# Optimization experiments

Hardware: AMD Instinct MI355X
Metric: run time of the kernel (lower is better)

The kernel has to match this reference:

```python
import jax, jax.numpy as jnp
import numpy as np

EPS = 1e-10
B, S, D, K = 8, 2048, 512, 1024
TEMP = 1.0  # quantizer temperature set to 1.0 in SQVAE.__init__


def _ln(x, g, b):
    m = x.mean(-1, keepdims=True)
    v = x.var(-1, keepdims=True)
    return (x - m) / jnp.sqrt(v + 1e-5) * g + b


def _mlp(x, w1, b1, g1, be1, w2, b2, g2, be2):
    # feed_forward: Linear -> ReLU -> LayerNorm, twice (MLPLayers=2)
    h = _ln(jax.nn.relu(x @ w1 + b1), g1, be1)
    return _ln(jax.nn.relu(h @ w2 + b2), g2, be2)


def setup_inputs() -> dict:
    key = jax.random.key(0)
    ks = jax.random.split(key, 20)
    W = 0.04  # small init scale to keep distances / softmax well-conditioned
    p = lambda k, sh, s=1.0: jax.random.normal(k, sh, dtype=jnp.float32) * s
    return {
        'x': p(ks[0], (B, S, D)),
        'gumbel_u': jax.random.uniform(ks[1], (B * S, K), dtype=jnp.float32),
        'enc_w1': p(ks[2], (D, D), W), 'enc_b1': jnp.zeros(D, jnp.float32),
        'enc_g1': jnp.ones(D, jnp.float32), 'enc_be1': jnp.zeros(D, jnp.float32),
        'enc_w2': p(ks[3], (D, D), W), 'enc_b2': jnp.zeros(D, jnp.float32),
        'enc_g2': jnp.ones(D, jnp.float32), 'enc_be2': jnp.zeros(D, jnp.float32),
        'dec_w1': p(ks[4], (D, D), W), 'dec_b1': jnp.zeros(D, jnp.float32),
        'dec_g1': jnp.ones(D, jnp.float32), 'dec_be1': jnp.zeros(D, jnp.float32),
        'dec_w2': p(ks[5], (D, D), W), 'dec_b2': jnp.zeros(D, jnp.float32),
        'dec_g2': jnp.ones(D, jnp.float32), 'dec_be2': jnp.zeros(D, jnp.float32),
        'codebook': p(ks[6], (K, D)),
        'log_param_q': jnp.zeros((), jnp.float32),
    }


def reference(x, gumbel_u, enc_w1, enc_b1, enc_g1, enc_be1, enc_w2, enc_b2, enc_g2, enc_be2,
              dec_w1, dec_b1, dec_g1, dec_be1, dec_w2, dec_b2, dec_g2, dec_be2,
              codebook, log_param_q):
    bs, seq, d = x.shape
    z = _mlp(x, enc_w1, enc_b1, enc_g1, enc_be1, enc_w2, enc_b2, enc_g2, enc_be2)
    # gaussian_1: log_var_q = 0 -> var_q = exp(log_param_q_scalar)
    var_q = jnp.exp(log_param_q)
    w = 0.5 / jnp.clip(var_q, 1e-10)  # 0.5 * precision_q (scalar)
    zf = z.reshape(-1, d)  # [N, D]
    # cdist^2 style distance, scaled by weight -> logits [N, K]
    dist = w * (jnp.sum(zf * zf, axis=1, keepdims=True)
                + jnp.sum(codebook * codebook, axis=1)
                - 2.0 * zf @ codebook.T)
    logit = -dist
    logp = jax.nn.log_softmax(logit, axis=-1)
    probs = jnp.exp(logp)
    # gumbel-softmax sample (train path), noise provided as uniform input
    g = -jnp.log(-jnp.log(gumbel_u + EPS) + EPS)
    encodings = jax.nn.softmax((logit + g) / TEMP, axis=-1)
    z_q = (encodings @ codebook).reshape(bs, seq, d)
    kld_discrete = jnp.sum(probs * logp) / bs
    kld_continuous = jnp.mean(jnp.sum((z - z_q) ** 2 * w, axis=(1, 2)))
    loss = kld_discrete + kld_continuous
    avg_probs = jnp.mean(jax.lax.stop_gradient(probs), axis=0)
    perplexity = jnp.exp(-jnp.sum(avg_probs * jnp.log(avg_probs + 1e-7)))
    x_rec = _mlp(z_q, dec_w1, dec_b1, dec_g1, dec_be1, dec_w2, dec_b2, dec_g2, dec_be2)
    return x_rec, loss, perplexity
```

## Files before the change

### kernel.cpp

```cpp
#include <hip/hip_runtime.h>
#include <math.h>

#define NROWS 16384
#define DIM   512
#define KCODE 1024

typedef __attribute__((ext_vector_type(8))) __bf16 bf16x8;
typedef __attribute__((ext_vector_type(4))) float f32x4;

__device__ __forceinline__ float wave_reduce_sum(float v) {
  #pragma unroll
  for (int m = 1; m < 64; m <<= 1) v += __shfl_xor(v, m, 64);
  return v;
}
__device__ __forceinline__ float wave_reduce_max(float v) {
  #pragma unroll
  for (int m = 1; m < 64; m <<= 1) v = fmaxf(v, __shfl_xor(v, m, 64));
  return v;
}
__device__ __forceinline__ unsigned short f2bf(float f) {
  union { float f; unsigned u; } v; v.f = f;
  unsigned r = v.u + 0x7FFFu + ((v.u >> 16) & 1u);
  return (unsigned short)(r >> 16);
}
__device__ __forceinline__ float bf2f(unsigned short h) {
  union { unsigned u; float f; } v; v.u = ((unsigned)h) << 16;
  return v.f;
}
__device__ __forceinline__ uint4 pack8(const float* x) {
  uint4 r;
  r.x = (unsigned)f2bf(x[0]) | ((unsigned)f2bf(x[1]) << 16);
  r.y = (unsigned)f2bf(x[2]) | ((unsigned)f2bf(x[3]) << 16);
  r.z = (unsigned)f2bf(x[4]) | ((unsigned)f2bf(x[5]) << 16);
  r.w = (unsigned)f2bf(x[6]) | ((unsigned)f2bf(x[7]) << 16);
  return r;
}

__device__ __forceinline__ void glds16(const void* g, void* lds) {
  __builtin_amdgcn_global_load_lds(
      (const __attribute__((address_space(1))) unsigned int*)g,
      (__attribute__((address_space(3))) unsigned int*)lds, 16, 0, 0);
}

template <int NPASS, int EPI, int K, int N, int LDA, int MROWS>
__global__ __launch_bounds__(512, 2) void gemm256(
    const unsigned short* A0, const unsigned short* A1, const unsigned short* A2,
    const unsigned short* B0, const unsigned short* B1, const unsigned short* B2,
    const float* __restrict__ znorm, const float* __restrict__ cnorm,
    const float* __restrict__ lpq,
    const unsigned short* __restrict__ zh, const unsigned short* __restrict__ zl,
    float* __restrict__ kldc,
    unsigned short* __restrict__ outb, float* __restrict__ outf) {
  __shared__ char smem[65536];
  const int t = threadIdx.x;
  const int l = t & 63, w = t >> 6;
  const int wm = w >> 2, wn = w & 3;
  const int NTN = N / 256;
  const int b = blockIdx.x;
  const int xcd = b & 7, j = b >> 3;
  const int MT_PER_XCD = (MROWS / 256) / 8;
  const int m0 = (xcd * MT_PER_XCD + j / NTN) * 256;
  const int n0 = (j % NTN) * 256;

  f32x4 acc[8][4];
  #pragma unroll
  for (int i = 0; i < 8; ++i)
    #pragma unroll
    for (int jj = 0; jj < 4; ++jj) acc[i][jj] = (f32x4){0.f, 0.f, 0.f, 0.f};

  const int row_lo = w * 16 + (l & 15);
  const int row_hi = (w + 8) * 16 + (l & 15);
  const int kcol = (l >> 4) * 8;
  const int dA0 = w * 1024;
  const int dA1 = (w + 8) * 1024;
  const int dB0 = 16384 + w * 1024;
  const int dB1 = 16384 + (w + 8) * 1024;

  const size_t oA0 = (size_t)(m0 + row_lo) * LDA + kcol;
  const size_t oA1 = (size_t)(m0 + row_hi) * LDA + kcol;
  const size_t oB0 = (size_t)(n0 + row_lo) * K + kcol;
  const size_t oB1 = (size_t)(n0 + row_hi) * K + kcol;

  constexpr int SPP = K / 32;
  constexpr int NSTEP = NPASS * SPP;

  auto issue = [&](int ss) {
    const int p = (NPASS == 1) ? 0 : (ss / SPP);
    const int kt = (ss % SPP) * 32;
    const unsigned short* A = (p == 0) ? A0 : (p == 1) ? A1 : A2;
    const unsigned short* B = (p == 0) ? B0 : (p == 1) ? B1 : B2;
    char* hb = smem + (ss & 1) * 32768;
    glds16(A + oA0 + kt, hb + dA0);
    glds16(A + oA1 + kt, hb + dA1);
    glds16(B + oB0 + kt, hb + dB0);
    glds16(B + oB1 + kt, hb + dB1);
  };

  issue(0);
  #pragma unroll 1
  for (int s = 0; s < NSTEP; ++s) {
    if (s + 1 < NSTEP) {
      issue(s + 1);
      asm volatile("s_waitcnt vmcnt(4)" ::: "memory");
    } else {
      asm volatile("s_waitcnt vmcnt(0)" ::: "memory");
    }
    __builtin_amdgcn_s_barrier();
    const char* hb = smem + (s & 1) * 32768;
    bf16x8 af[8], bfr[4];
    #pragma unroll
    for (int i = 0; i < 4; ++i)
      bfr[i] = *(const bf16x8*)(hb + 16384 + (wn * 4 + i) * 1024 + l * 16);
    #pragma unroll
    for (int i = 0; i < 8; ++i)
      af[i] = *(const bf16x8*)(hb + (wm * 8 + i) * 1024 + l * 16);
    #pragma unroll
    for (int mi = 0; mi < 8; ++mi)
      #pragma unroll
      for (int ni = 0; ni < 4; ++ni)
        acc[mi][ni] = __builtin_amdgcn_mfma_f32_16x16x32_bf16(af[mi], bfr[ni], acc[mi][ni], 0, 0, 0);
    __builtin_amdgcn_s_barrier();
  }

  float* slab = (float*)(smem + w * 4352);
  const int q = l >> 4, c16 = l & 15;
  const int c4 = (l & 15) * 4;
  const float wq = 0.5f / fmaxf(expf(lpq[0]), 1e-10f);
  float local = 0.f;

  #pragma unroll
  for (int mi = 0; mi < 8; ++mi) {
    __syncthreads();
    #pragma unroll
    for (int ni = 0; ni < 4; ++ni)
      #pragma unroll
      for (int r = 0; r < 4; ++r)
        slab[(q * 4 + r) * 68 + ni * 16 + c16] = acc[mi][ni][r];
    __syncthreads();
    #pragma unroll
    for (int pp = 0; pp < 4; ++pp) {
      const int row = pp * 4 + q;
      const float4 v4 = *(const float4*)&slab[row * 68 + c4];
      float v[4] = {v4.x, v4.y, v4.z, v4.w};
      const int m = m0 + wm * 128 + mi * 16 + row;
      const int nc = n0 + wn * 64 + c4;
      if (EPI == 1) {
        const float zn = znorm[m];
        const float4 cn = *(const float4*)&cnorm[nc];
        float4 o;
        o.x = -wq * (zn + cn.x - 2.f * v[0]);
        o.y = -wq * (zn + cn.y - 2.f * v[1]);
        o.z = -wq * (zn + cn.z - 2.f * v[2]);
        o.w = -wq * (zn + cn.w - 2.f * v[3]);
        *(float4*)&outf[(size_t)m * N + nc] = o;
      } else {
        const uint2 h2 = *(const uint2*)&zh[(size_t)m * N + nc];
        const uint2 l2 = *(const uint2*)&zl[(size_t)m * N + nc];
        const float z0 = bf2f((unsigned short)(h2.x & 0xFFFF)) + bf2f((unsigned short)(l2.x & 0xFFFF));
        const float z1 = bf2f((unsigned short)(h2.x >> 16))    + bf2f((unsigned short)(l2.x >> 16));
        const float z2 = bf2f((unsigned short)(h2.y & 0xFFFF)) + bf2f((unsigned short)(l2.y & 0xFFFF));
        const float z3 = bf2f((unsigned short)(h2.y >> 16))    + bf2f((unsigned short)(l2.y >> 16));
        const float d0 = z0 - v[0], d1 = z1 - v[1], d2 = z2 - v[2], d3 = z3 - v[3];
        local += d0 * d0 + d1 * d1 + d2 * d2 + d3 * d3;
        uint2 st;
        st.x = (unsigned)f2bf(v[0]) | ((unsigned)f2bf(v[1]) << 16);
        st.y = (unsigned)f2bf(v[2]) | ((unsigned)f2bf(v[3]) << 16);
        *(uint2*)&outb[(size_t)m * N + nc] = st;
      }
    }
  }
  if (EPI == 2) {
    local = wave_reduce_sum(local) * wq;
    if (l == 0) atomicAdd(kldc, local);
  }
}

template <int NPASS, int EPI, int K, int N, int LDA>
__global__ __launch_bounds__(256) void gemm_bt(
    const unsigned short* A0, const unsigned short* A1, const unsigned short* A2,
    const unsigned short* B0, const unsigned short* B1, const unsigned short* B2,
    const float* __restrict__ bias,
    const float* __restrict__ znorm, const float* __restrict__ cnorm,
    const float* __restrict__ lpq,
    const unsigned short* __restrict__ zh, const unsigned short* __restrict__ zl,
    float* __restrict__ kldc,
    unsigned short* __restrict__ outb, float* __restrict__ outf) {
  __shared__ char smem[32768];
  const int t = threadIdx.x;
  const int l = t & 63, w = t >> 6;
  const int wm = w >> 1, wn = w & 1;
  const int NTN = N / 128;
  const int b = blockIdx.x;
  const int xcd = b & 7;
  const int j = b >> 3;
  const int m0 = (xcd * 16 + j / NTN) * 128;
  const int n0 = (j % NTN) * 128;

  f32x4 acc[4][4];
  #pragma unroll
  for (int i = 0; i < 4; ++i)
    #pragma unroll
    for (int jj = 0; jj < 4; ++jj) acc[i][jj] = (f32x4){0.f, 0.f, 0.f, 0.f};

  const int row_lo = w * 16 + (l & 15);
  const int row_hi = (w + 4) * 16 + (l & 15);
  const int kcol = (l >> 4) * 8;
  const int dA0 = w * 1024;
  const int dA1 = (w + 4) * 1024;
  const int dB0 = 8192 + w * 1024;
  const int dB1 = 8192 + (w + 4) * 1024;

  const size_t oA0 = (size_t)(m0 + row_lo) * LDA + kcol;
  const size_t oA1 = (size_t)(m0 + row_hi) * LDA + kcol;
  const size_t oB0 = (size_t)(n0 + row_lo) * K + kcol;
  const size_t oB1 = (size_t)(n0 + row_hi) * K + kcol;

  constexpr int SPP = K / 32;
  constexpr int NSTEP = NPASS * SPP;

  auto issue = [&](int ss) {
    const int p = (NPASS == 1) ? 0 : (ss / SPP);
    const int kt = (ss % SPP) * 32;
    const unsigned short* A = (p == 0) ? A0 : (p == 1) ? A1 : A2;
    const unsigned short* B = (p == 0) ? B0 : (p == 1) ? B1 : B2;
    char* hb = smem + (ss & 1) * 16384;
    glds16(A + oA0 + kt, hb + dA0);
    glds16(A + oA1 + kt, hb + dA1);
    glds16(B + oB0 + kt, hb + dB0);
    glds16(B + oB1 + kt, hb + dB1);
  };

  issue(0);
  #pragma unroll 1
  for (int s = 0; s < NSTEP; ++s) {
    if (s + 1 < NSTEP) {
      issue(s + 1);
      asm volatile("s_waitcnt vmcnt(4)" ::: "memory");
    } else {
      asm volatile("s_waitcnt vmcnt(0)" ::: "memory");
    }
    __builtin_amdgcn_s_barrier();
    const char* hb = smem + (s & 1) * 16384;
    bf16x8 af[4], bfr[4];
    #pragma unroll
    for (int i = 0; i < 4; ++i) {
      af[i]  = *(const bf16x8*)(hb + (wm * 4 + i) * 1024 + l * 16);
      bfr[i] = *(const bf16x8*)(hb + 8192 + (wn * 4 + i) * 1024 + l * 16);
    }
    #pragma unroll
    for (int mi = 0; mi < 4; ++mi)
      #pragma unroll
      for (int ni = 0; ni < 4; ++ni)
        acc[mi][ni] = __builtin_amdgcn_mfma_f32_16x16x32_bf16(af[mi], bfr[ni], acc[mi][ni], 0, 0, 0);
    __builtin_amdgcn_s_barrier();
  }

  float* slab = (float*)(smem + w * 4352);
  const int q = l >> 4, c16 = l & 15;
  const int c4 = (l & 15) * 4;
  const float wq = (EPI >= 1) ? 0.5f / fmaxf(expf(lpq[0]), 1e-10f) : 0.f;
  float local = 0.f;

  #pragma unroll
  for (int mi = 0; mi < 4; ++mi) {
    __syncthreads();
    #pragma unroll
    for (int ni = 0; ni < 4; ++ni)
      #pragma unroll
      for (int r = 0; r < 4; ++r)
        slab[(q * 4 + r) * 68 + ni * 16 + c16] = acc[mi][ni][r];
    __syncthreads();
    #pragma unroll
    for (int pp = 0; pp < 4; ++pp) {
      const int row = pp * 4 + q;
      const float4 v4 = *(const float4*)&slab[row * 68 + c4];
      float v[4] = {v4.x, v4.y, v4.z, v4.w};
      const int m = m0 + wm * 64 + mi * 16 + row;
      const int nc = n0 + wn * 64 + c4;
      if (EPI == 0) {
        const float4 b4 = *(const float4*)&bias[nc];
        v[0] = fmaxf(v[0] + b4.x, 0.f);
        v[1] = fmaxf(v[1] + b4.y, 0.f);
        v[2] = fmaxf(v[2] + b4.z, 0.f);
        v[3] = fmaxf(v[3] + b4.w, 0.f);
        uint2 st;
        st.x = (unsigned)f2bf(v[0]) | ((unsigned)f2bf(v[1]) << 16);
        st.y = (unsigned)f2bf(v[2]) | ((unsigned)f2bf(v[3]) << 16);
        *(uint2*)&outb[(size_t)m * N + nc] = st;
      } else if (EPI == 1) {
        const float zn = znorm[m];
        const float4 cn = *(const float4*)&cnorm[nc];
        float4 o;
        o.x = -wq * (zn + cn.x - 2.f * v[0]);
        o.y = -wq * (zn + cn.y - 2.f * v[1]);
        o.z = -wq * (zn + cn.z - 2.f * v[2]);
        o.w = -wq * (zn + cn.w - 2.f * v[3]);
        *(float4*)&outf[(size_t)m * N + nc] = o;
      } else {
        const uint2 h2 = *(const uint2*)&zh[(size_t)m * N + nc];
        const uint2 l2 = *(const uint2*)&zl[(size_t)m * N + nc];
        const float z0 = bf2f((unsigned short)(h2.x & 0xFFFF)) + bf2f((unsigned short)(l2.x & 0xFFFF));
        const float z1 = bf2f((unsigned short)(h2.x >> 16))    + bf2f((unsigned short)(l2.x >> 16));
        const float z2 = bf2f((unsigned short)(h2.y & 0xFFFF)) + bf2f((unsigned short)(l2.y & 0xFFFF));
        const float z3 = bf2f((unsigned short)(h2.y >> 16))    + bf2f((unsigned short)(l2.y >> 16));
        const float d0 = z0 - v[0], d1 = z1 - v[1], d2 = z2 - v[2], d3 = z3 - v[3];
        local += d0 * d0 + d1 * d1 + d2 * d2 + d3 * d3;
        uint2 st;
        st.x = (unsigned)f2bf(v[0]) | ((unsigned)f2bf(v[1]) << 16);
        st.y = (unsigned)f2bf(v[2]) | ((unsigned)f2bf(v[3]) << 16);
        *(uint2*)&outb[(size_t)m * N + nc] = st;
      }
    }
  }
  if (EPI == 2) {
    local = wave_reduce_sum(local) * wq;
    if (l == 0) atomicAdd(kldc, local);
  }
}

template <int MODE>
__global__ __launch_bounds__(256) void ln_rows(
    const unsigned short* __restrict__ X, const float* __restrict__ g,
    const float* __restrict__ be, unsigned short* __restrict__ Y,
    unsigned short* __restrict__ Yl, float* __restrict__ znorm,
    float* __restrict__ Yf) {
  const int l = threadIdx.x & 63, wv = threadIdx.x >> 6;
  float gv[8], bv[8];
  {
    const float4 a = *(const float4*)&g[l * 8];
    const float4 b = *(const float4*)&g[l * 8 + 4];
    gv[0] = a.x; gv[1] = a.y; gv[2] = a.z; gv[3] = a.w;
    gv[4] = b.x; gv[5] = b.y; gv[6] = b.z; gv[7] = b.w;
    const float4 c = *(const float4*)&be[l * 8];
    const float4 d = *(const float4*)&be[l * 8 + 4];
    bv[0] = c.x; bv[1] = c.y; bv[2] = c.z; bv[3] = c.w;
    bv[4] = d.x; bv[5] = d.y; bv[6] = d.z; bv[7] = d.w;
  }
  const int row0 = blockIdx.x * 32 + wv * 8;
  for (int rr = 0; rr < 8; ++rr) {
    const int row = row0 + rr;
    const uint4 raw = *(const uint4*)&X[(size_t)row * 512 + l * 8];
    float v[8];
    const unsigned rw[4] = {raw.x, raw.y, raw.z, raw.w};
    #pragma unroll
    for (int i = 0; i < 4; ++i) {
      v[2 * i]     = bf2f((unsigned short)(rw[i] & 0xFFFF));
      v[2 * i + 1] = bf2f((unsigned short)(rw[i] >> 16));
    }
    float s = 0.f, ss = 0.f;
    #pragma unroll
    for (int i = 0; i < 8; ++i) { s += v[i]; ss += v[i] * v[i]; }
    #pragma unroll
    for (int m = 1; m < 64; m <<= 1) {
      s += __shfl_xor(s, m, 64);
      ss += __shfl_xor(ss, m, 64);
    }
    const float mean = s * (1.f / 512.f);
    const float var = ss * (1.f / 512.f) - mean * mean;
    const float rstd = rsqrtf(var + 1e-5f);
    float y[8];
    #pragma unroll
    for (int i = 0; i < 8; ++i) y[i] = (v[i] - mean) * rstd * gv[i] + bv[i];
    if (MODE == 0) {
      *(uint4*)&Y[(size_t)row * 512 + l * 8] = pack8(y);
    } else if (MODE == 1) {
      float lo[8], ns = 0.f;
      unsigned short hx[8];
      #pragma unroll
      for (int i = 0; i < 8; ++i) {
        hx[i] = f2bf(y[i]);
        lo[i] = y[i] - bf2f(hx[i]);
        ns += y[i] * y[i];
      }
      uint4 hv;
      hv.x = (unsigned)hx[0] | ((unsigned)hx[1] << 16);
      hv.y = (unsigned)hx[2] | ((unsigned)hx[3] << 16);
      hv.z = (unsigned)hx[4] | ((unsigned)hx[5] << 16);
      hv.w = (unsigned)hx[6] | ((unsigned)hx[7] << 16);
      *(uint4*)&Y[(size_t)row * 512 + l * 8] = hv;
      *(uint4*)&Yl[(size_t)row * 512 + l * 8] = pack8(lo);
      ns = wave_reduce_sum(ns);
      if (l == 0) znorm[row] = ns;
    } else {
      float4 o0, o1;
      o0.x = y[0]; o0.y = y[1]; o0.z = y[2]; o0.w = y[3];
      o1.x = y[4]; o1.y = y[5]; o1.z = y[6]; o1.w = y[7];
      *(float4*)&Yf[(size_t)row * 512 + l * 8] = o0;
      *(float4*)&Yf[(size_t)row * 512 + l * 8 + 4] = o1;
    }
  }
}

__global__ __launch_bounds__(256) void convert_f32_bf16(
    const float* __restrict__ X, unsigned short* __restrict__ Y) {
  const size_t i = ((size_t)blockIdx.x * 256 + threadIdx.x) * 8;
  const float4 a = *(const float4*)&X[i];
  const float4 b = *(const float4*)&X[i + 4];
  float v[8] = {a.x, a.y, a.z, a.w, b.x, b.y, b.z, b.w};
  *(uint4*)&Y[i] = pack8(v);
}

__global__ __launch_bounds__(256) void prep_cb(
    const float* __restrict__ CB, unsigned short* __restrict__ H,
    unsigned short* __restrict__ L, float* __restrict__ cnorm) {
  const int wv = threadIdx.x >> 6, l = threadIdx.x & 63;
  const int r = blockIdx.x * 4 + wv;
  const float* row = &CB[(size_t)r * 512 + l * 8];
  const float4 a = *(const float4*)row;
  const float4 b = *(const float4*)(row + 4);
  float x[8] = {a.x, a.y, a.z, a.w, b.x, b.y, b.z, b.w};
  float s = 0.f, lo[8];
  unsigned short hi[8];
  #pragma unroll
  for (int i = 0; i < 8; ++i) {
    s += x[i] * x[i];
    hi[i] = f2bf(x[i]);
    lo[i] = x[i] - bf2f(hi[i]);
  }
  uint4 hv;
  hv.x = (unsigned)hi[0] | ((unsigned)hi[1] << 16);
  hv.y = (unsigned)hi[2] | ((unsigned)hi[3] << 16);
  hv.z = (unsigned)hi[4] | ((unsigned)hi[5] << 16);
  hv.w = (unsigned)hi[6] | ((unsigned)hi[7] << 16);
  *(uint4*)&H[(size_t)r * 512 + l * 8] = hv;
  *(uint4*)&L[(size_t)r * 512 + l * 8] = pack8(lo);
  s = wave_reduce_sum(s);
  if (l == 0) cnorm[r] = s;
}

__global__ __launch_bounds__(256) void transpose_f32_bf16(
    const float* __restrict__ in, unsigned short* __restrict__ out, int R, int C) {
  __shared__ float tile[32][33];
  const int ntc = C >> 5;
  const int c0 = (blockIdx.x % ntc) * 32, r0 = (blockIdx.x / ntc) * 32;
  const int tx = threadIdx.x & 31, ty = threadIdx.x >> 5;
  #pragma unroll
  for (int i = 0; i < 4; ++i)
    tile[ty + 8 * i][tx] = in[(size_t)(r0 + ty + 8 * i) * C + c0 + tx];
  __syncthreads();
  #pragma unroll
  for (int i = 0; i < 4; ++i)
    out[(size_t)(c0 + ty + 8 * i) * R + r0 + tx] = f2bf(tile[tx][ty + 8 * i]);
}

__global__ __launch_bounds__(256) void softmax_gumbel(
    const float* logits, const float* __restrict__ U, unsigned short* E,
    float* __restrict__ colsum, float* __restrict__ kldd_acc) {
  __shared__ float cs[1024];
  __shared__ float kd[4];
  const int t = threadIdx.x;
  const int wv = t >> 6, l = t & 63;
  #pragma unroll
  for (int i = 0; i < 4; ++i) cs[t + 256 * i] = 0.f;
  __syncthreads();
  float psum[16];
  #pragma unroll
  for (int i = 0; i < 16; ++i) psum[i] = 0.f;
  float kldd = 0.f;
  const int nbase = blockIdx.x * 16 + wv * 4;

  for (int it = 0; it < 4; ++it) {
    const int row = nbase + it;
    const size_t off = (size_t)row * KCODE + 4 * l;
    float v[16];
    #pragma unroll
    for (int jj = 0; jj < 4; ++jj) {
      const float4 t4 = *(const float4*)&logits[off + 256 * jj];
      v[4 * jj + 0] = t4.x; v[4 * jj + 1] = t4.y; v[4 * jj + 2] = t4.z; v[4 * jj + 3] = t4.w;
    }
    float m = v[0];
    #pragma unroll
    for (int i = 1; i < 16; ++i) m = fmaxf(m, v[i]);
    m = wave_reduce_max(m);
    float se = 0.f;
    #pragma unroll
    for (int i = 0; i < 16; ++i) se += expf(v[i] - m);
    se = wave_reduce_sum(se);
    const float lz = logf(se);
    float pl = 0.f;
    #pragma unroll
    for (int i = 0; i < 16; ++i) {
      const float lp = v[i] - m - lz;
      const float p = expf(lp);
      psum[i] += p;
      pl += p * lp;
    }
    kldd += pl;
    float y[16];
    #pragma unroll
    for (int jj = 0; jj < 4; ++jj) {
      const float4 t4 = *(const float4*)&U[off + 256 * jj];
      y[4 * jj + 0] = v[4 * jj + 0] - logf(-logf(t4.x + 1e-10f) + 1e-10f);
      y[4 * jj + 1] = v[4 * jj + 1] - logf(-logf(t4.y + 1e-10f) + 1e-10f);
      y[4 * jj + 2] = v[4 * jj + 2] - logf(-logf(t4.z + 1e-10f) + 1e-10f);
      y[4 * jj + 3] = v[4 * jj + 3] - logf(-logf(t4.w + 1e-10f) + 1e-10f);
    }
    float m2 = y[0];
    #pragma unroll
    for (int i = 1; i < 16; ++i) m2 = fmaxf(m2, y[i]);
    m2 = wave_reduce_max(m2);
    float s2 = 0.f;
    #pragma unroll
    for (int i = 0; i < 16; ++i) s2 += expf(y[i] - m2);
    s2 = wave_reduce_sum(s2);
    const float inv = 1.f / s2;
    #pragma unroll
    for (int jj = 0; jj < 4; ++jj) {
      ushort4 e;
      e.x = f2bf(expf(y[4 * jj + 0] - m2) * inv);
      e.y = f2bf(expf(y[4 * jj + 1] - m2) * inv);
      e.z = f2bf(expf(y[4 * jj + 2] - m2) * inv);
      e.w = f2bf(expf(y[4 * jj + 3] - m2) * inv);
      *(ushort4*)&E[(size_t)row * 2048 + 4 * l + 256 * jj] = e;
    }
  }
  #pragma unroll
  for (int jj = 0; jj < 4; ++jj)
    #pragma unroll
    for (int c = 0; c < 4; ++c)
      atomicAdd(&cs[256 * jj + 4 * l + c], psum[4 * jj + c]);
  kldd = wave_reduce_sum(kldd);
  if (l == 0) kd[wv] = kldd;
  __syncthreads();
  #pragma unroll
  for (int i = 0; i < 4; ++i) {
    const float vv = cs[t + 256 * i];
    if (vv != 0.f) atomicAdd(&colsum[t + 256 * i], vv);
  }
  if (t == 0) atomicAdd(kldd_acc, kd[0] + kd[1] + kd[2] + kd[3]);
}

__global__ __launch_bounds__(256) void finalize(
    const float* __restrict__ colsum, const float* __restrict__ scal,
    float* __restrict__ out) {
  const int t = threadIdx.x;
  float ent = 0.f;
  #pragma unroll
  for (int jj = 0; jj < 4; ++jj) {
    const float a = colsum[t + 256 * jj] * (1.f / 16384.f);
    ent += a * logf(a + 1e-7f);
  }
  ent = wave_reduce_sum(ent);
  __shared__ float red[4];
  if ((t & 63) == 0) red[t >> 6] = ent;
  __syncthreads();
  if (t == 0) {
    const float tot = red[0] + red[1] + red[2] + red[3];
    out[0] = (scal[0] + scal[1]) * (1.f / 8.f);
    out[1] = expf(-tot);
  }
}

extern "C" void kernel_launch(void* const* d_in, const int* in_sizes, int n_in,
                              void* d_out, int out_size, void* d_ws, size_t ws_size,
                              hipStream_t stream) {
  const float* x      = (const float*)d_in[0];
  const float* gu     = (const float*)d_in[1];
  const float* enc_w1 = (const float*)d_in[2];
  const float* enc_b1 = (const float*)d_in[3];
  const float* enc_g1 = (const float*)d_in[4];
  const float* enc_e1 = (const float*)d_in[5];
  const float* enc_w2 = (const float*)d_in[6];
  const float* enc_b2 = (const float*)d_in[7];
  const float* enc_g2 = (const float*)d_in[8];
  const float* enc_e2 = (const float*)d_in[9];
  const float* dec_w1 = (const float*)d_in[10];
  const float* dec_b1 = (const float*)d_in[11];
  const float* dec_g1 = (const float*)d_in[12];
  const float* dec_e1 = (const float*)d_in[13];
  const float* dec_w2 = (const float*)d_in[14];
  const float* dec_b2 = (const float*)d_in[15];
  const float* dec_g2 = (const float*)d_in[16];
  const float* dec_e2 = (const float*)d_in[17];
  const float* cb     = (const float*)d_in[18];
  const float* lpq    = (const float*)d_in[19];
  float* out = (float*)d_out;
  char* wsb = (char*)d_ws;

  float*          logits = (float*)(wsb + 0);
  unsigned short* Eb     = (unsigned short*)(wsb + 0);
  unsigned short* t1     = (unsigned short*)(wsb + 67108864);
  unsigned short* xb     = (unsigned short*)(wsb + 83886080);
  unsigned short* zh     = xb;
  unsigned short* hq     = (unsigned short*)(wsb + 100663296);
  unsigned short* zl     = (unsigned short*)(wsb + 117440512);
  unsigned short* wt0    = (unsigned short*)(wsb + 134217728);
  unsigned short* wt1    = wt0 + 262144;
  unsigned short* wt2    = wt1 + 262144;
  unsigned short* wt3    = wt2 + 262144;
  unsigned short* cbh    = (unsigned short*)(wsb + 136314880);
  unsigned short* cbl    = (unsigned short*)(wsb + 137363456);
  unsigned short* cbT    = (unsigned short*)(wsb + 138412032);
  float*          znorm  = (float*)(wsb + 139460608);
  float*          cnorm  = (float*)(wsb + 139526144);
  float*          colsum = (float*)(wsb + 139530240);
  float*          scal   = (float*)(wsb + 139534336);

  hipMemsetAsync(colsum, 0, 4096 + 16, stream);

  convert_f32_bf16<<<4096, 256, 0, stream>>>(x, xb);
  prep_cb<<<256, 256, 0, stream>>>(cb, cbh, cbl, cnorm);
  transpose_f32_bf16<<<256, 256, 0, stream>>>(enc_w1, wt0, 512, 512);
  transpose_f32_bf16<<<256, 256, 0, stream>>>(enc_w2, wt1, 512, 512);
  transpose_f32_bf16<<<256, 256, 0, stream>>>(dec_w1, wt2, 512, 512);
  transpose_f32_bf16<<<256, 256, 0, stream>>>(dec_w2, wt3, 512, 512);
  transpose_f32_bf16<<<512, 256, 0, stream>>>(cb, cbT, 1024, 512);

  gemm_bt<1, 0, 512, 512, 512><<<512, 256, 0, stream>>>(
      xb, nullptr, nullptr, wt0, nullptr, nullptr, enc_b1,
      nullptr, nullptr, nullptr, nullptr, nullptr, nullptr, t1, nullptr);
  ln_rows<0><<<512, 256, 0, stream>>>(t1, enc_g1, enc_e1, hq, nullptr, nullptr, nullptr);
  gemm_bt<1, 0, 512, 512, 512><<<512, 256, 0, stream>>>(
      hq, nullptr, nullptr, wt1, nullptr, nullptr, enc_b2,
      nullptr, nullptr, nullptr, nullptr, nullptr, nullptr, t1, nullptr);
  ln_rows<1><<<512, 256, 0, stream>>>(t1, enc_g2, enc_e2, zh, zl, znorm, nullptr);
  gemm256<3, 1, 512, 1024, 512, 16384><<<256, 512, 0, stream>>>(
      zh, zl, zh, cbh, cbh, cbl,
      znorm, cnorm, lpq, nullptr, nullptr, nullptr, nullptr, logits);
  softmax_gumbel<<<1024, 256, 0, stream>>>(logits, gu, Eb, colsum, &scal[0]);
  gemm256<1, 2, 1024, 512, 2048, 16384><<<128, 512, 0, stream>>>(
      Eb, nullptr, nullptr, cbT, nullptr, nullptr,
      nullptr, nullptr, lpq, zh, zl, &scal[1], hq, nullptr);
  gemm_bt<1, 0, 512, 512, 512><<<512, 256, 0, stream>>>(
      hq, nullptr, nullptr, wt2, nullptr, nullptr, dec_b1,
      nullptr, nullptr, nullptr, nullptr, nullptr, nullptr, t1, nullptr);
  ln_rows<0><<<512, 256, 0, stream>>>(t1, dec_g1, dec_e1, zl, nullptr, nullptr, nullptr);
  gemm_bt<1, 0, 512, 512, 512><<<512, 256, 0, stream>>>(
      zl, nullptr, nullptr, wt3, nullptr, nullptr, dec_b2,
      nullptr, nullptr, nullptr, nullptr, nullptr, nullptr, t1, nullptr);
  ln_rows<2><<<512, 256, 0, stream>>>(t1, dec_g2, dec_e2, nullptr, nullptr, nullptr, out);
  finalize<<<1, 256, 0, stream>>>(colsum, scal, out + 8388608);
}
```

Baseline: 523.1 us.

## Fuse split-bf16 distance GEMM passes into single kernel sharing LDS tiles

Replaces the three-pass gemm256 distance GEMM (zh*cbh, zh*cbl, zl*cbh) with a dedicated kernel that loads zh, zl, cbh and cbl tiles together into a double-buffered 128KB LDS and does all three MFMA products per k-step. Operand tiles are reused across passes, cutting redundant global loads and loop overhead. The larger LDS footprint (128KB) may reduce occupancy below the declared 2 blocks per CU.

```diff
diff --git a/kernel.cpp b/kernel.cpp
--- a/kernel.cpp
+++ b/kernel.cpp
@@ -40,6 +40,116 @@
   __builtin_amdgcn_global_load_lds(
       (const __attribute__((address_space(1))) unsigned int*)g,
       (__attribute__((address_space(3))) unsigned int*)lds, 16, 0, 0);
+}
+
+__global__ __launch_bounds__(512, 2) void dist_fused(
+    const unsigned short* __restrict__ zhp, const unsigned short* __restrict__ zlp,
+    const unsigned short* __restrict__ cbh, const unsigned short* __restrict__ cbl,
+    const float* __restrict__ znorm, const float* __restrict__ cnorm,
+    const float* __restrict__ lpq, float* __restrict__ outf) {
+  __shared__ char smem[131072];
+  const int t = threadIdx.x;
+  const int l = t & 63, w = t >> 6;
+  const int wm = w >> 2, wn = w & 3;
+  const int b = blockIdx.x;
+  const int xcd = b & 7, j = b >> 3;
+  const int m0 = (xcd * 8 + j / 4) * 256;
+  const int n0 = (j % 4) * 256;
+
+  f32x4 acc[8][4];
+  #pragma unroll
+  for (int i = 0; i < 8; ++i)
+    #pragma unroll
+    for (int jj = 0; jj < 4; ++jj) acc[i][jj] = (f32x4){0.f, 0.f, 0.f, 0.f};
+
+  const int row = l & 15;
+  const int kcol = (l >> 4) * 8;
+  const size_t aLo = (size_t)(m0 + w * 16 + row) * 512 + kcol;
+  const size_t aHi = aLo + (size_t)128 * 512;
+  const size_t bLo = (size_t)(n0 + w * 16 + row) * 512 + kcol;
+  const size_t bHi = bLo + (size_t)128 * 512;
+
+  auto issue = [&](int s) {
+    char* hb = smem + (s & 1) * 65536;
+    const int kt = s * 32;
+    glds16(zhp + aLo + kt, hb + w * 1024);
+    glds16(zhp + aHi + kt, hb + (w + 8) * 1024);
+    glds16(zlp + aLo + kt, hb + 16384 + w * 1024);
+    glds16(zlp + aHi + kt, hb + 16384 + (w + 8) * 1024);
+    glds16(cbh + bLo + kt, hb + 32768 + w * 1024);
+    glds16(cbh + bHi + kt, hb + 32768 + (w + 8) * 1024);
+    glds16(cbl + bLo + kt, hb + 49152 + w * 1024);
+    glds16(cbl + bHi + kt, hb + 49152 + (w + 8) * 1024);
+  };
+
+  issue(0);
+  #pragma unroll 1
+  for (int s = 0; s < 16; ++s) {
+    if (s + 1 < 16) {
+      issue(s + 1);
+      asm volatile("s_waitcnt vmcnt(8)" ::: "memory");
+    } else {
+      asm volatile("s_waitcnt vmcnt(0)" ::: "memory");
+    }
+    __builtin_amdgcn_s_barrier();
+    const char* hb = smem + (s & 1) * 65536;
+    bf16x8 af[8], bh[4], bl_[4];
+    #pragma unroll
+    for (int i = 0; i < 4; ++i) {
+      bh[i]  = *(const bf16x8*)(hb + 32768 + (wn * 4 + i) * 1024 + l * 16);
+      bl_[i] = *(const bf16x8*)(hb + 49152 + (wn * 4 + i) * 1024 + l * 16);
+    }
+    #pragma unroll
+    for (int i = 0; i < 8; ++i)
+      af[i] = *(const bf16x8*)(hb + (wm * 8 + i) * 1024 + l * 16);
+    #pragma unroll
+    for (int mi = 0; mi < 8; ++mi)
+      #pragma unroll
+      for (int ni = 0; ni < 4; ++ni) {
+        acc[mi][ni] = __builtin_amdgcn_mfma_f32_16x16x32_bf16(af[mi], bh[ni], acc[mi][ni], 0, 0, 0);
+        acc[mi][ni] = __builtin_amdgcn_mfma_f32_16x16x32_bf16(af[mi], bl_[ni], acc[mi][ni], 0, 0, 0);
+      }
+    #pragma unroll
+    for (int i = 0; i < 8; ++i)
+      af[i] = *(const bf16x8*)(hb + 16384 + (wm * 8 + i) * 1024 + l * 16);
+    #pragma unroll
+    for (int mi = 0; mi < 8; ++mi)
+      #pragma unroll
+      for (int ni = 0; ni < 4; ++ni)
+        acc[mi][ni] = __builtin_amdgcn_mfma_f32_16x16x32_bf16(af[mi], bh[ni], acc[mi][ni], 0, 0, 0);
+    __builtin_amdgcn_s_barrier();
+  }
+
+  float* slab = (float*)(smem + w * 4352);
+  const int q = l >> 4, c16 = l & 15;
+  const int c4 = (l & 15) * 4;
+  const float wq = 0.5f / fmaxf(expf(lpq[0]), 1e-10f);
+
+  #pragma unroll
+  for (int mi = 0; mi < 8; ++mi) {
+    __syncthreads();
+    #pragma unroll
+    for (int ni = 0; ni < 4; ++ni)
+      #pragma unroll
+      for (int r = 0; r < 4; ++r)
+        slab[(q * 4 + r) * 68 + ni * 16 + c16] = acc[mi][ni][r];
+    __syncthreads();
+    #pragma unroll
+    for (int pp = 0; pp < 4; ++pp) {
+      const int rw = pp * 4 + q;
+      const float4 v4 = *(const float4*)&slab[rw * 68 + c4];
+      const int m = m0 + wm * 128 + mi * 16 + rw;
+      const int nc = n0 + wn * 64 + c4;
+      const float zn = znorm[m];
+      const float4 cn = *(const float4*)&cnorm[nc];
+      float4 o;
+      o.x = -wq * (zn + cn.x - 2.f * v4.x);
+      o.y = -wq * (zn + cn.y - 2.f * v4.y);
+      o.z = -wq * (zn + cn.z - 2.f * v4.z);
+      o.w = -wq * (zn + cn.w - 2.f * v4.w);
+      *(float4*)&outf[(size_t)m * KCODE + nc] = o;
+    }
+  }
 }
 
 template <int NPASS, int EPI, int K, int N, int LDA, int MROWS>
@@ -139,10 +249,10 @@
     __syncthreads();
     #pragma unroll
     for (int pp = 0; pp < 4; ++pp) {
-      const int row = pp * 4 + q;
-      const float4 v4 = *(const float4*)&slab[row * 68 + c4];
+      const int rw = pp * 4 + q;
+      const float4 v4 = *(const float4*)&slab[rw * 68 + c4];
       float v[4] = {v4.x, v4.y, v4.z, v4.w};
-      const int m = m0 + wm * 128 + mi * 16 + row;
+      const int m = m0 + wm * 128 + mi * 16 + rw;
       const int nc = n0 + wn * 64 + c4;
       if (EPI == 1) {
         const float zn = znorm[m];
@@ -272,10 +382,10 @@
     __syncthreads();
     #pragma unroll
     for (int pp = 0; pp < 4; ++pp) {
-      const int row = pp * 4 + q;
-      const float4 v4 = *(const float4*)&slab[row * 68 + c4];
+      const int rw = pp * 4 + q;
+      const float4 v4 = *(const float4*)&slab[rw * 68 + c4];
       float v[4] = {v4.x, v4.y, v4.z, v4.w};
-      const int m = m0 + wm * 64 + mi * 16 + row;
+      const int m = m0 + wm * 64 + mi * 16 + rw;
       const int nc = n0 + wn * 64 + c4;
       if (EPI == 0) {
         const float4 b4 = *(const float4*)&bias[nc];
@@ -614,9 +724,8 @@
       hq, nullptr, nullptr, wt1, nullptr, nullptr, enc_b2,
       nullptr, nullptr, nullptr, nullptr, nullptr, nullptr, t1, nullptr);
   ln_rows<1><<<512, 256, 0, stream>>>(t1, enc_g2, enc_e2, zh, zl, znorm, nullptr);
-  gemm256<3, 1, 512, 1024, 512, 16384><<<256, 512, 0, stream>>>(
-      zh, zl, zh, cbh, cbh, cbl,
-      znorm, cnorm, lpq, nullptr, nullptr, nullptr, nullptr, logits);
+  dist_fused<<<256, 512, 0, stream>>>(
+      zh, zl, cbh, cbl, znorm, cnorm, lpq, logits);
   softmax_gumbel<<<1024, 256, 0, stream>>>(logits, gu, Eb, colsum, &scal[0]);
   gemm256<1, 2, 1024, 512, 2048, 16384><<<128, 512, 0, stream>>>(
       Eb, nullptr, nullptr, cbT, nullptr, nullptr,
```

Result: faster. 463.1 us (-11.5%).
